# Kernel optimization log

Measured on AMD Instinct MI355X. Metric: run time of the kernel, lower is better.

Reference implementation:

```python
import jax, jax.numpy as jnp
import numpy as np

NQ = 16  # nqubits
BATCH = 256

def _ry(t):
    # t: (...,) real angles -> (..., 2, 2) complex64 Ry(t)
    c = jnp.cos(t / 2).astype(jnp.complex64)
    s = jnp.sin(t / 2).astype(jnp.complex64)
    return jnp.stack([jnp.stack([c, -s], -1), jnp.stack([s, c], -1)], -2)

def _rz(t):
    # diag(e^{-i t/2}, e^{i t/2})
    e0 = jnp.exp(-0.5j * t.astype(jnp.complex64))
    e1 = jnp.exp(0.5j * t.astype(jnp.complex64))
    z = jnp.zeros_like(e0)
    return jnp.stack([jnp.stack([e0, z], -1), jnp.stack([z, e1], -1)], -2)

def _apply_1q(st, g, w):
    # st: (B, 2^n) complex, g: (2,2) or (B,2,2); wire w (0 = most significant, matching kron order)
    B = st.shape[0]
    x = st.reshape(B, 2 ** w, 2, -1)
    if g.ndim == 3:
        x = jnp.einsum('iab,ilbr->ilar', g, x)
    else:
        x = jnp.einsum('ab,ilbr->ilar', g, x)
    return x.reshape(B, -1)

def _apply_cnot(st, c, t, n):
    # CNOT(control=c, target=t): flip target bit where control bit == 1
    B = st.shape[0]
    x = st.reshape((B,) + (2,) * n)
    c_ax = c + 1
    ctrl0 = jnp.take(x, 0, axis=c_ax)
    ctrl1 = jnp.take(x, 1, axis=c_ax)
    t_ax = t + 1 if t < c else t  # target axis index after removing control axis
    ctrl1 = jnp.flip(ctrl1, axis=t_ax)  # flip along size-2 axis == Pauli-X
    x = jnp.stack([ctrl0, ctrl1], axis=c_ax)
    return x.reshape(B, -1)

def _yzy(st, w3, n):
    # per-qubit Ry(a) Rz(b) Ry(c); params laid out (n, 3) applied in order a, b, c
    p = w3.reshape(n, 3)
    g = jnp.einsum('nab,nbc,ncd->nad', _ry(p[:, 2]), _rz(p[:, 1]), _ry(p[:, 0]))
    for i in range(n):
        st = _apply_1q(st, g[i], i)
    return st

def _ring(st, step, n):
    # ring_of_cnot (step=1) / ring_of_cnot2 (step=2)
    for i in range(n):
        st = _apply_cnot(st, i, (i + step) % n, n)
    return st

def _forward(inputs, weight):
    B, n = inputs.shape
    # |0...0> initial state, batched
    st = jnp.zeros((B, 2 ** n), jnp.complex64).at[:, 0].set(1.0)
    # PauliEncoding with pauli='Y': Ry(inputs[:, i]) on wire i (batched gate)
    enc = _ry(inputs)  # (B, n, 2, 2)
    for i in range(n):
        st = _apply_1q(st, enc[:, i], i)
    # BasicEntangleLayer x2 = YZY + ring_of_cnot
    st = _yzy(st, weight[0 * n:3 * n], n); st = _ring(st, 1, n)
    st = _yzy(st, weight[3 * n:6 * n], n); st = _ring(st, 1, n)
    # YZY, ring_of_cnot2, YZY, ring_of_cnot2, YZY
    st = _yzy(st, weight[6 * n:9 * n], n); st = _ring(st, 2, n)
    st = _yzy(st, weight[9 * n:12 * n], n); st = _ring(st, 2, n)
    st = _yzy(st, weight[12 * n:15 * n], n)
    # <Z_i> = sum_probs(bit_i=0) - sum_probs(bit_i=1); output scaled by 4 as in original
    probs = st.real ** 2 + st.imag ** 2  # (B, 2^n) real
    z = []
    for i in range(n):
        p = probs.reshape(B, 2 ** i, 2, -1)
        z.append((p[:, :, 0, :] - p[:, :, 1, :]).sum(axis=(1, 2)))
    return jnp.stack(z, axis=1) * 4.0  # (B, n)

def setup_inputs() -> dict:
    key = jax.random.key(0)
    k1, k2 = jax.random.split(key)
    inputs = jax.random.uniform(k1, (BATCH, NQ), jnp.float32, 0.0, 2.0 * np.pi)
    weight = jax.random.uniform(k2, (15 * NQ,), jnp.float32, 0.0, 2.0 * np.pi)
    return {"inputs": inputs, "weight": weight}

def reference(inputs, weight):
    return _forward(inputs, weight)
```

## Files before the change

### kernel.cpp

```cpp
#include <hip/hip_runtime.h>
#include <hip/hip_fp16.h>
#include <utility>
#include <type_traits>


struct M16 { unsigned r[16]; };

constexpr M16 ident() { M16 m{}; for (int i = 0; i < 16; ++i) m.r[i] = 1u << i; return m; }

constexpr M16 ringm(int s) {
  M16 m = ident();
  for (int i = 15; i >= 0; --i) {
    int pc = 15 - i;
    int pt = 15 - ((i + s) & 15);
    m.r[pt] ^= m.r[pc];
  }
  return m;
}

constexpr M16 mmul(M16 A, M16 B) {
  M16 C{};
  for (int p = 0; p < 16; ++p) {
    unsigned v = 0;
    for (int q = 0; q < 16; ++q) if ((A.r[p] >> q) & 1u) v ^= B.r[q];
    C.r[p] = v;
  }
  return C;
}

constexpr M16 minv(M16 A) {
  M16 I = ident();
  for (int col = 0; col < 16; ++col) {
    int piv = -1;
    for (int row = col; row < 16; ++row) if ((A.r[row] >> col) & 1u) { piv = row; break; }
    unsigned t = A.r[piv]; A.r[piv] = A.r[col]; A.r[col] = t;
    t = I.r[piv]; I.r[piv] = I.r[col]; I.r[col] = t;
    for (int row = 0; row < 16; ++row)
      if (row != col && ((A.r[row] >> col) & 1u)) { A.r[row] ^= A.r[col]; I.r[row] ^= I.r[col]; }
  }
  return I;
}

constexpr bool meq(M16 a, M16 b) { for (int i = 0; i < 16; ++i) if (a.r[i] != b.r[i]) return false; return true; }
constexpr unsigned colmask(M16 P, int b) { unsigned m = 0; for (int p = 0; p < 16; ++p) m |= ((P.r[p] >> b) & 1u) << p; return m; }
constexpr int popc16(unsigned x) { int c = 0; for (int i = 0; i < 16; ++i) c += (x >> i) & 1; return c; }
constexpr int topbit_pow(unsigned x) { int b = 0; for (int i = 0; i < 16; ++i) if ((x >> i) & 1) b = i; return 1 << b; }

struct Tables { unsigned gm[64]; unsigned gc[64]; unsigned meas[16]; };

constexpr Tables make_tables() {
  Tables T{};
  M16 R1 = ringm(1), R2 = ringm(2);
  M16 P0 = R1;
  M16 P1 = mmul(R1, R1);
  M16 P2 = mmul(P1, R2);
  M16 P3 = mmul(P2, R2);
  M16 P[4] = { P0, P1, P2, P3 };
  for (int k = 0; k < 4; ++k) {
    M16 A = minv(P[k]);
    for (int b = 0; b < 16; ++b) {
      T.gm[k * 16 + b] = colmask(P[k], b);
      T.gc[k * 16 + b] = A.r[b];
    }
  }
  M16 A5 = minv(P[3]);
  for (int w = 0; w < 16; ++w) T.meas[w] = A5.r[15 - w];
  return T;
}

constexpr Tables TB = make_tables();

constexpr bool check_tables() {
  for (int g = 0; g < 64; ++g) if ((popc16(TB.gm[g] & TB.gc[g]) & 1) != 1) return false;
  if (!meq(mmul(ringm(1), minv(ringm(1))), ident())) return false;
  if (!meq(mmul(ringm(2), minv(ringm(2))), ident())) return false;
  return true;
}
static_assert(check_tables(), "GF(2) table inconsistency");
static_assert(sizeof(__half2) == 4, "half2 size");

template<int N, int I = 0, typename F>
__device__ __forceinline__ void sfor(F&& f) {
  if constexpr (I < N) {
    f(std::integral_constant<int, I>{});
    sfor<N, I + 1>(static_cast<F&&>(f));
  }
}

__device__ __forceinline__ int h2i(__half2 v) { return __builtin_bit_cast(int, v); }
__device__ __forceinline__ __half2 i2h(int v) { return __builtin_bit_cast(__half2, v); }
__device__ __forceinline__ unsigned h2u(__half2 v) { return __builtin_bit_cast(unsigned, v); }
__device__ __forceinline__ __half2 u2h(unsigned v) { return __builtin_bit_cast(__half2, v); }

__device__ __forceinline__ __half2 hswap(__half2 v) { __half2 r; r.x = v.y; r.y = v.x; return r; }

__device__ __forceinline__ __half2 updc(__half2 xs, __half2 xp, const __half2 (&s)[4]) {
  __half2 y = __hmul2(s[0], xs);
  y = __hfma2(s[1], hswap(xs), y);
  y = __hfma2(s[2], xp, y);
  y = __hfma2(s[3], hswap(xp), y);
  return y;
}
template<int T>
__device__ __forceinline__ __half2 upd(__half2 xs, __half2 xp,
                                       const __half2 (&s0)[4], const __half2 (&s1)[4]) {
  if constexpr (T) return updc(xs, xp, s1); else return updc(xs, xp, s0);
}

__device__ __forceinline__ void su2_coeffs(float a, float b, float c,
                                           float& are, float& aim, float& bre, float& bim) {
  float sapc, capc, samc, camc, sb, cb;
  __sincosf((a + c) * 0.5f, &sapc, &capc);
  __sincosf((a - c) * 0.5f, &samc, &camc);
  __sincosf(b * 0.5f, &sb, &cb);
  are = cb * capc;
  aim = -sb * camc;
  bre = cb * sapc;
  bim = sb * samc;
}

__device__ __forceinline__ unsigned pkh2(float lo, float hi) {
  return h2u(__floats2half2_rn(lo, hi));
}

__device__ __forceinline__ float2 cmulf(float2 a, float vr, float vi) {
  return make_float2(a.x * vr - a.y * vi, a.x * vi + a.y * vr);
}

template<int G>
__device__ __forceinline__ void apply_gate(__half2 (&S)[64], unsigned tid,
                                           const unsigned* ctab, unsigned* xbuf) {
  constexpr unsigned m  = TB.gm[G];
  constexpr unsigned c  = TB.gc[G];
  constexpr unsigned mL = m & 63u;
  constexpr unsigned mT = m >> 6;
  constexpr unsigned mW = m >> 12;
  constexpr int      dt = popc16(c & mL) & 1;

  __half2 s0[4], s1[4];
  {
    const unsigned f = __popc((c >> 6) & tid) & 1u;
#pragma unroll
    for (int q = 0; q < 4; ++q) {
      const unsigned lo = ctab[G * 8 + q];
      const unsigned hi = ctab[G * 8 + 4 + q];
      s0[q] = u2h(f ? hi : lo);
      s1[q] = u2h(f ? lo : hi);
    }
  }

  if constexpr (mT == 0u) {
    static_assert(mT != 0u || dt == 1, "register-pair gate must flip role locally");
    constexpr int hb = topbit_pow(mL);
    sfor<32>([&](auto ii) {
      constexpr int i  = decltype(ii)::value;
      constexpr int L0 = ((i & ~(hb - 1)) << 1) | (i & (hb - 1));
      constexpr int L1 = L0 ^ (int)mL;
      constexpr int t  = popc16(c & (unsigned)L0) & 1;
      const __half2 x0 = S[L0], x1 = S[L1];
      S[L0] = upd<t>(x0, x1, s0, s1);
      S[L1] = upd<t ^ dt>(x1, x0, s0, s1);
    });
  } else if constexpr (mW == 0u) {
    if constexpr (mL == 0u) {
      sfor<64>([&](auto ll) {
        constexpr int L = decltype(ll)::value;
        constexpr int t = popc16(c & (unsigned)L) & 1;
        const __half2 xp = i2h(__shfl_xor(h2i(S[L]), (int)mT, 64));
        S[L] = upd<t>(S[L], xp, s0, s1);
      });
    } else {
      constexpr int hb = topbit_pow(mL);
      sfor<32>([&](auto ii) {
        constexpr int i  = decltype(ii)::value;
        constexpr int L0 = ((i & ~(hb - 1)) << 1) | (i & (hb - 1));
        constexpr int L1 = L0 ^ (int)mL;
        constexpr int t  = popc16(c & (unsigned)L0) & 1;
        const __half2 x0 = S[L0], x1 = S[L1];
        const __half2 xp0 = i2h(__shfl_xor(h2i(x1), (int)mT, 64));
        const __half2 xp1 = i2h(__shfl_xor(h2i(x0), (int)mT, 64));
        S[L0] = upd<t>(x0, xp0, s0, s1);
        S[L1] = upd<t ^ dt>(x1, xp1, s0, s1);
      });
    }
  } else {
    constexpr unsigned hc = mL >> 3;
    const unsigned ptid = tid ^ mT;
    if constexpr (hc == 0u) {
      sfor<4>([&](auto gg_) {
        constexpr int g = decltype(gg_)::value;
        sfor<16>([&](auto ss) {
          constexpr int s = decltype(ss)::value;
          xbuf[s * 1024 + tid] = h2u(S[g * 16 + s]);
        });
        __syncthreads();
        sfor<16>([&](auto ss) {
          constexpr int s    = decltype(ss)::value;
          constexpr int L    = g * 16 + s;
          constexpr int slot = (L ^ (int)mL) & 15;
          constexpr int t    = popc16(c & (unsigned)L) & 1;
          const __half2 xp = u2h(xbuf[slot * 1024 + ptid]);
          S[L] = upd<t>(S[L], xp, s0, s1);
        });
        __syncthreads();
      });
    } else {
      constexpr int tb = topbit_pow(hc);
      sfor<8>([&](auto cc) {
        constexpr int cA = decltype(cc)::value;
        if constexpr ((cA & tb) == 0) {
          constexpr int cB = cA ^ (int)hc;
          sfor<8>([&](auto ss) {
            constexpr int s = decltype(ss)::value;
            xbuf[s * 1024 + tid]       = h2u(S[cA * 8 + s]);
            xbuf[(8 + s) * 1024 + tid] = h2u(S[cB * 8 + s]);
          });
          __syncthreads();
          sfor<8>([&](auto ss) {
            constexpr int s = decltype(ss)::value;
            {
              constexpr int L    = cA * 8 + s;
              constexpr int slot = 8 + ((L ^ (int)mL) & 7);
              constexpr int t    = popc16(c & (unsigned)L) & 1;
              const __half2 xp = u2h(xbuf[slot * 1024 + ptid]);
              S[L] = upd<t>(S[L], xp, s0, s1);
            }
            {
              constexpr int L    = cB * 8 + s;
              constexpr int slot = (L ^ (int)mL) & 7;
              constexpr int t    = popc16(c & (unsigned)L) & 1;
              const __half2 xp = u2h(xbuf[slot * 1024 + ptid]);
              S[L] = upd<t>(S[L], xp, s0, s1);
            }
          });
          __syncthreads();
        }
      });
    }
  }
}

__global__ __launch_bounds__(1024, 4)
void qcir_kernel(const float* __restrict__ inputs, const float* __restrict__ weight,
                 float* __restrict__ out) {
  __shared__ unsigned xbuf[24 * 1024];
  __shared__ unsigned ctab[64 * 8];
  __shared__ float4   itab[16];
  __shared__ float    red[16 * 16];

  const unsigned tid = threadIdx.x;
  const unsigned b   = blockIdx.x;

  if (tid < 64) {
    const int g = (int)tid;
    const int k = g >> 4;
    const int bb = g & 15;
    const int w = 15 - bb;
    const int base = 48 * (k + 1) + 3 * w;
    float are, aim, bre, bim;
    su2_coeffs(weight[base], weight[base + 1], weight[base + 2], are, aim, bre, bim);
    ctab[g * 8 + 0] = pkh2(are, are);
    ctab[g * 8 + 1] = pkh2(-aim, aim);
    ctab[g * 8 + 2] = pkh2(-bre, -bre);
    ctab[g * 8 + 3] = pkh2(-bim, bim);
    ctab[g * 8 + 4] = pkh2(are, are);
    ctab[g * 8 + 5] = pkh2(aim, -aim);
    ctab[g * 8 + 6] = pkh2(bre, bre);
    ctab[g * 8 + 7] = pkh2(-bim, bim);
  } else if (tid < 80) {
    const int w = (int)tid - 64;
    const float a = weight[3 * w] + inputs[b * 16 + w];
    float are, aim, bre, bim;
    su2_coeffs(a, weight[3 * w + 1], weight[3 * w + 2], are, aim, bre, bim);
    itab[w] = make_float4(are, aim, bre, bim);
  }
  __syncthreads();

  __half2 S[64];
  float2 P = make_float2(1.f, 0.f);
#pragma unroll
  for (int p = 6; p <= 15; ++p) {
    const int bit = (int)(tid >> (p - 6)) & 1;
    const float4 t = itab[15 - p];
    P = cmulf(P, bit ? t.z : t.x, bit ? t.w : t.y);
  }
  sfor<8>([&](auto hh) {
    constexpr int h = decltype(hh)::value;
    float2 ph = P;
    sfor<3>([&](auto qq) {
      constexpr int q   = decltype(qq)::value;
      constexpr int bit = (h >> q) & 1;
      const float4 t = itab[15 - (3 + q)];
      if constexpr (bit) ph = cmulf(ph, t.z, t.w); else ph = cmulf(ph, t.x, t.y);
    });
    sfor<8>([&](auto ll) {
      constexpr int l = decltype(ll)::value;
      float2 pl = ph;
      sfor<3>([&](auto qq) {
        constexpr int q   = decltype(qq)::value;
        constexpr int bit = (l >> q) & 1;
        const float4 t = itab[15 - q];
        if constexpr (bit) pl = cmulf(pl, t.z, t.w); else pl = cmulf(pl, t.x, t.y);
      });
      S[h * 8 + l] = __floats2half2_rn(pl.x, pl.y);
    });
  });

  sfor<64>([&](auto gg) { apply_gate<decltype(gg)::value>(S, tid, ctab, xbuf); });

  float acc[16];
  sfor<16>([&](auto ww) { acc[decltype(ww)::value] = 0.f; });
  sfor<64>([&](auto ll) {
    constexpr int L = decltype(ll)::value;
    const float re = __low2float(S[L]);
    const float im = __high2float(S[L]);
    const float p = re * re + im * im;
    sfor<16>([&](auto ww) {
      constexpr int w = decltype(ww)::value;
      constexpr int t = popc16(TB.meas[w] & 63u & (unsigned)L) & 1;
      if constexpr (t) acc[w] -= p; else acc[w] += p;
    });
  });
  sfor<16>([&](auto ww) {
    constexpr int w = decltype(ww)::value;
    const unsigned fw = __popc((TB.meas[w] >> 6) & tid) & 1u;
    float z = fw ? -acc[w] : acc[w];
#pragma unroll
    for (int d = 1; d < 64; d <<= 1) z += __shfl_xor(z, d, 64);
    if ((tid & 63u) == 0u) red[(tid >> 6) * 16 + w] = z;
  });
  __syncthreads();
  if (tid < 16) {
    float s = 0.f;
#pragma unroll
    for (int v = 0; v < 16; ++v) s += red[v * 16 + tid];
    out[b * 16 + tid] = 4.f * s;
  }
}

extern "C" void kernel_launch(void* const* d_in, const int* in_sizes, int n_in,
                              void* d_out, int out_size, void* d_ws, size_t ws_size,
                              hipStream_t stream) {
  const float* inputs = (const float*)d_in[0];
  const float* weight = (const float*)d_in[1];
  float* out = (float*)d_out;
  const int B = in_sizes[0] / 16;
  qcir_kernel<<<B, 1024, 0, stream>>>(inputs, weight, out);
}
```

Baseline: 337.1 us.

## Split state between registers and LDS with compile-time qubit remapping

Each thread now keeps half its 64 amplitudes in registers and half in a resident LDS array. The split uses a compile-time permutation of qubits to physical bit positions, chosen greedily so most gates are local or touch only the LDS half. Cross-wave gates now read and update the partner amplitudes in place in LDS instead of staging them through an exchange buffer. This aims to cut register pressure and the exchange traffic, but adds LDS accesses to every gate and a barrier before most non-local gates. It also drops the occupancy hint in the launch bounds and halves the coefficient table by applying the sign flip with an XOR.

```diff
diff --git a/kernel.cpp b/kernel.cpp
--- a/kernel.cpp
+++ b/kernel.cpp
@@ -45,6 +45,7 @@
 constexpr unsigned colmask(M16 P, int b) { unsigned m = 0; for (int p = 0; p < 16; ++p) m |= ((P.r[p] >> b) & 1u) << p; return m; }
 constexpr int popc16(unsigned x) { int c = 0; for (int i = 0; i < 16; ++i) c += (x >> i) & 1; return c; }
 constexpr int topbit_pow(unsigned x) { int b = 0; for (int i = 0; i < 16; ++i) if ((x >> i) & 1) b = i; return 1 << b; }
+constexpr int ctzu(unsigned x) { for (int i = 0; i < 32; ++i) if ((x >> i) & 1) return i; return 32; }
 
 struct Tables { unsigned gm[64]; unsigned gc[64]; unsigned meas[16]; };
 
@@ -79,6 +80,104 @@
 static_assert(check_tables(), "GF(2) table inconsistency");
 static_assert(sizeof(__half2) == 4, "half2 size");
 
+struct Assign {
+  int hpos; unsigned wset, rset, lset;
+  int nbad;
+  int phys_of[16];
+  int orig_of[16];
+  unsigned pm[64], pc[64], pmeas[16];
+};
+
+constexpr Assign make_assign() {
+  Assign A{};
+  int bestBad = 1000, bh = -1; unsigned bw = 0;
+  for (int h = 0; h < 16; ++h) {
+    bool alive[64]; int nAlive = 0;
+    for (int g = 0; g < 64; ++g) {
+      alive[g] = ((TB.gm[g] >> h) & 1u) == 0u;
+      if (alive[g]) ++nAlive;
+    }
+    unsigned w = 0;
+    int covered = 0;
+    for (int pick = 0; pick < 4; ++pick) {
+      int bestP = -1, bestC = -1;
+      for (int p = 0; p < 16; ++p) {
+        if (p == h || ((w >> p) & 1u)) continue;
+        int cnt = 0;
+        for (int g = 0; g < 64; ++g)
+          if (alive[g] && ((TB.gm[g] >> p) & 1u)) ++cnt;
+        if (cnt > bestC) { bestC = cnt; bestP = p; }
+      }
+      w |= 1u << bestP;
+      for (int g = 0; g < 64; ++g)
+        if (alive[g] && ((TB.gm[g] >> bestP) & 1u)) { alive[g] = false; ++covered; }
+    }
+    int bad = covered;
+    if (bad < bestBad) { bestBad = bad; bh = h; bw = w; }
+  }
+  A.hpos = bh; A.wset = bw; A.nbad = bestBad;
+
+  unsigned rem = 0xFFFFu & ~bw & ~(1u << bh);
+  int pos[11] = {}; int np = 0;
+  for (int p = 0; p < 16; ++p) if ((rem >> p) & 1u) pos[np++] = p;
+  int bestLoc = -1; unsigned br = 0;
+  for (int a = 0; a < 11; ++a) for (int b = a + 1; b < 11; ++b)
+    for (int c = b + 1; c < 11; ++c) for (int d = c + 1; d < 11; ++d)
+      for (int e = d + 1; e < 11; ++e) {
+        unsigned r = (1u << pos[a]) | (1u << pos[b]) | (1u << pos[c]) | (1u << pos[d]) | (1u << pos[e]);
+        unsigned localset = r | (1u << bh);
+        int loc = 0;
+        for (int g = 0; g < 64; ++g) if ((TB.gm[g] & ~localset) == 0u) ++loc;
+        if (loc > bestLoc) { bestLoc = loc; br = r; }
+      }
+  A.rset = br; A.lset = rem & ~br;
+
+  int pr = 0, pl = 6, pw = 12;
+  for (int p = 0; p < 16; ++p) {
+    if ((A.rset >> p) & 1u)      { A.phys_of[p] = pr;  A.orig_of[pr]  = p; ++pr; }
+    else if (p == bh)            { A.phys_of[p] = 5;   A.orig_of[5]   = p; }
+    else if ((A.lset >> p) & 1u) { A.phys_of[p] = pl;  A.orig_of[pl]  = p; ++pl; }
+    else                         { A.phys_of[p] = pw;  A.orig_of[pw]  = p; ++pw; }
+  }
+  for (int g = 0; g < 64; ++g) {
+    unsigned m = 0, c = 0;
+    for (int p = 0; p < 16; ++p) {
+      if ((TB.gm[g] >> p) & 1u) m |= 1u << A.phys_of[p];
+      if ((TB.gc[g] >> p) & 1u) c |= 1u << A.phys_of[p];
+    }
+    A.pm[g] = m; A.pc[g] = c;
+  }
+  for (int w2 = 0; w2 < 16; ++w2) {
+    unsigned mm = 0;
+    for (int p = 0; p < 16; ++p) if ((TB.meas[w2] >> p) & 1u) mm |= 1u << A.phys_of[p];
+    A.pmeas[w2] = mm;
+  }
+  return A;
+}
+
+constexpr Assign AS = make_assign();
+
+constexpr bool check_assign() {
+  for (int g = 0; g < 64; ++g) if ((popc16(AS.pm[g] & AS.pc[g]) & 1) != 1) return false;
+  if (popc16(AS.rset) != 5 || popc16(AS.wset) != 4 || popc16(AS.lset) != 6) return false;
+  return true;
+}
+static_assert(check_assign(), "assignment inconsistency");
+
+struct RPlan { int stage[32]; int slot[32]; };
+constexpr RPlan make_rplan(unsigned mr) {
+  RPlan P{}; bool vis[32] = {};
+  int g = 0, sl = 0;
+  for (int r = 0; r < 32; ++r) if (!vis[r]) {
+    int p = r ^ (int)mr;
+    P.stage[r] = g; P.slot[r] = sl; vis[r] = true; ++sl;
+    if (p != r) { P.stage[p] = g; P.slot[p] = sl; vis[p] = true; ++sl; }
+    if (sl >= 4) { sl = 0; ++g; }
+  }
+  return P;
+}
+template<unsigned MR> constexpr RPlan rplan_v = make_rplan(MR);
+
 template<int N, int I = 0, typename F>
 __device__ __forceinline__ void sfor(F&& f) {
   if constexpr (I < N) {
@@ -94,17 +193,18 @@
 
 __device__ __forceinline__ __half2 hswap(__half2 v) { __half2 r; r.x = v.y; r.y = v.x; return r; }
 
-__device__ __forceinline__ __half2 updc(__half2 xs, __half2 xp, const __half2 (&s)[4]) {
-  __half2 y = __hmul2(s[0], xs);
-  y = __hfma2(s[1], hswap(xs), y);
-  y = __hfma2(s[2], xp, y);
+template<int T>
+__device__ __forceinline__ __half2 upd(__half2 x, __half2 xp, const __half2 (&s)[4]) {
+  __half2 y = __hmul2(s[0], x);
+  if constexpr (T) {
+    y = __hfma2(__hneg2(s[1]), hswap(x), y);
+    y = __hfma2(__hneg2(s[2]), xp, y);
+  } else {
+    y = __hfma2(s[1], hswap(x), y);
+    y = __hfma2(s[2], xp, y);
+  }
   y = __hfma2(s[3], hswap(xp), y);
   return y;
-}
-template<int T>
-__device__ __forceinline__ __half2 upd(__half2 xs, __half2 xp,
-                                       const __half2 (&s0)[4], const __half2 (&s1)[4]) {
-  if constexpr (T) return updc(xs, xp, s1); else return updc(xs, xp, s0);
 }
 
 __device__ __forceinline__ void su2_coeffs(float a, float b, float c,
@@ -128,123 +228,152 @@
 }
 
 template<int G>
-__device__ __forceinline__ void apply_gate(__half2 (&S)[64], unsigned tid,
-                                           const unsigned* ctab, unsigned* xbuf) {
-  constexpr unsigned m  = TB.gm[G];
-  constexpr unsigned c  = TB.gc[G];
-  constexpr unsigned mL = m & 63u;
-  constexpr unsigned mT = m >> 6;
-  constexpr unsigned mW = m >> 12;
-  constexpr int      dt = popc16(c & mL) & 1;
-
-  __half2 s0[4], s1[4];
-  {
-    const unsigned f = __popc((c >> 6) & tid) & 1u;
-#pragma unroll
-    for (int q = 0; q < 4; ++q) {
-      const unsigned lo = ctab[G * 8 + q];
-      const unsigned hi = ctab[G * 8 + 4 + q];
-      s0[q] = u2h(f ? hi : lo);
-      s1[q] = u2h(f ? lo : hi);
-    }
-  }
-
-  if constexpr (mT == 0u) {
-    static_assert(mT != 0u || dt == 1, "register-pair gate must flip role locally");
-    constexpr int hb = topbit_pow(mL);
-    sfor<32>([&](auto ii) {
-      constexpr int i  = decltype(ii)::value;
-      constexpr int L0 = ((i & ~(hb - 1)) << 1) | (i & (hb - 1));
-      constexpr int L1 = L0 ^ (int)mL;
-      constexpr int t  = popc16(c & (unsigned)L0) & 1;
-      const __half2 x0 = S[L0], x1 = S[L1];
-      S[L0] = upd<t>(x0, x1, s0, s1);
-      S[L1] = upd<t ^ dt>(x1, x0, s0, s1);
-    });
-  } else if constexpr (mW == 0u) {
-    if constexpr (mL == 0u) {
-      sfor<64>([&](auto ll) {
-        constexpr int L = decltype(ll)::value;
-        constexpr int t = popc16(c & (unsigned)L) & 1;
-        const __half2 xp = i2h(__shfl_xor(h2i(S[L]), (int)mT, 64));
-        S[L] = upd<t>(S[L], xp, s0, s1);
+__device__ __forceinline__ void apply_gate(__half2 (&R)[32], unsigned tid,
+                                           const unsigned* ctab, unsigned* ldsS,
+                                           unsigned* xbuf) {
+  constexpr unsigned m   = AS.pm[G];
+  constexpr unsigned c   = AS.pc[G];
+  constexpr unsigned mr  = m & 31u;
+  constexpr unsigned mh  = (m >> 5) & 1u;
+  constexpr unsigned mt  = (m >> 6) & 1023u;
+  constexpr unsigned mw  = m >> 12;
+  constexpr unsigned cr  = c & 31u;
+  constexpr unsigned chb = (c >> 5) & 1u;
+
+  const unsigned f  = __popc((c >> 6) & tid) & 1u;
+  const unsigned fm = f ? 0x80008000u : 0u;
+  __half2 s[4];
+  s[0] = u2h(ctab[G * 4 + 0]);
+  s[1] = u2h(ctab[G * 4 + 1] ^ fm);
+  s[2] = u2h(ctab[G * 4 + 2] ^ fm);
+  s[3] = u2h(ctab[G * 4 + 3]);
+
+  constexpr bool curLocal  = (m >> 6) == 0u;
+  constexpr bool prevLocal = (G == 0) ? true : ((AS.pm[G - 1] >> 6) == 0u);
+  if constexpr (!(curLocal && prevLocal)) __syncthreads();
+
+  if constexpr (mt == 0u) {
+    if constexpr (mh == 0u) {
+      constexpr int hb = topbit_pow(mr);
+      sfor<16>([&](auto ii) {
+        constexpr int i  = decltype(ii)::value;
+        constexpr int r0 = ((i & ~(hb - 1)) << 1) | (i & (hb - 1));
+        constexpr int r1 = r0 ^ (int)mr;
+        constexpr int t0 = popc16(cr & (unsigned)r0) & 1;
+        {
+          const __half2 x0 = R[r0], x1 = R[r1];
+          R[r0] = upd<t0>(x0, x1, s);
+          R[r1] = upd<t0 ^ 1>(x1, x0, s);
+        }
+        {
+          constexpr int tl = t0 ^ (int)chb;
+          const __half2 x0 = u2h(ldsS[r0 * 1024 + tid]);
+          const __half2 x1 = u2h(ldsS[r1 * 1024 + tid]);
+          ldsS[r0 * 1024 + tid] = h2u(upd<tl>(x0, x1, s));
+          ldsS[r1 * 1024 + tid] = h2u(upd<tl ^ 1>(x1, x0, s));
+        }
       });
     } else {
-      constexpr int hb = topbit_pow(mL);
-      sfor<32>([&](auto ii) {
-        constexpr int i  = decltype(ii)::value;
-        constexpr int L0 = ((i & ~(hb - 1)) << 1) | (i & (hb - 1));
-        constexpr int L1 = L0 ^ (int)mL;
-        constexpr int t  = popc16(c & (unsigned)L0) & 1;
-        const __half2 x0 = S[L0], x1 = S[L1];
-        const __half2 xp0 = i2h(__shfl_xor(h2i(x1), (int)mT, 64));
-        const __half2 xp1 = i2h(__shfl_xor(h2i(x0), (int)mT, 64));
-        S[L0] = upd<t>(x0, xp0, s0, s1);
-        S[L1] = upd<t ^ dt>(x1, xp1, s0, s1);
+      sfor<32>([&](auto rr) {
+        constexpr int r = decltype(rr)::value;
+        constexpr int t = popc16(cr & (unsigned)r) & 1;
+        const __half2 x = R[r];
+        const __half2 y = u2h(ldsS[(r ^ (int)mr) * 1024 + tid]);
+        R[r] = upd<t>(x, y, s);
+        ldsS[(r ^ (int)mr) * 1024 + tid] = h2u(upd<t ^ 1>(y, x, s));
       });
     }
+  } else if constexpr (mh == 1u) {
+    const unsigned pt = tid ^ mt;
+    sfor<32>([&](auto rr) {
+      constexpr int r = decltype(rr)::value;
+      constexpr int t = popc16(cr & (unsigned)r) & 1;
+      const __half2 x = R[r];
+      const __half2 y = u2h(ldsS[(r ^ (int)mr) * 1024 + pt]);
+      R[r] = upd<t>(x, y, s);
+      ldsS[(r ^ (int)mr) * 1024 + pt] = h2u(upd<t ^ 1>(y, x, s));
+    });
   } else {
-    constexpr unsigned hc = mL >> 3;
-    const unsigned ptid = tid ^ mT;
-    if constexpr (hc == 0u) {
-      sfor<4>([&](auto gg_) {
-        constexpr int g = decltype(gg_)::value;
-        sfor<16>([&](auto ss) {
-          constexpr int s = decltype(ss)::value;
-          xbuf[s * 1024 + tid] = h2u(S[g * 16 + s]);
+    const unsigned pt = tid ^ mt;
+    if constexpr (mr != 0u) {
+      constexpr int q = ctzu(mr);
+      sfor<32>([&](auto rr) {
+        constexpr int r = decltype(rr)::value;
+        if constexpr (((r >> q) & 1) == 0) {
+          constexpr int r2 = r ^ (int)mr;
+          constexpr int t  = (popc16(cr & (unsigned)r) & 1) ^ (int)chb;
+          const __half2 x = u2h(ldsS[r * 1024 + tid]);
+          const __half2 y = u2h(ldsS[r2 * 1024 + pt]);
+          ldsS[r * 1024 + tid] = h2u(upd<t>(x, y, s));
+          ldsS[r2 * 1024 + pt] = h2u(upd<t ^ 1>(y, x, s));
+        }
+      });
+    } else {
+      const unsigned po = (tid >> ctzu(mt)) & 1u;
+      sfor<32>([&](auto rr) {
+        constexpr int r  = decltype(rr)::value;
+        constexpr int r4 = (r >> 4) & 1;
+        constexpr int t  = (popc16(cr & (unsigned)r) & 1) ^ (int)chb;
+        if (po == (unsigned)r4) {
+          const __half2 x = u2h(ldsS[r * 1024 + tid]);
+          const __half2 y = u2h(ldsS[r * 1024 + pt]);
+          ldsS[r * 1024 + tid] = h2u(upd<t>(x, y, s));
+          ldsS[r * 1024 + pt]  = h2u(upd<t ^ 1>(y, x, s));
+        }
+      });
+    }
+    if constexpr (mw == 0u) {
+      if constexpr (mr == 0u) {
+        sfor<32>([&](auto rr) {
+          constexpr int r = decltype(rr)::value;
+          constexpr int t = popc16(cr & (unsigned)r) & 1;
+          const __half2 xp = i2h(__shfl_xor(h2i(R[r]), (int)mt, 64));
+          R[r] = upd<t>(R[r], xp, s);
+        });
+      } else {
+        constexpr int hb = topbit_pow(mr);
+        constexpr int dt = popc16(cr & mr) & 1;
+        sfor<16>([&](auto ii) {
+          constexpr int i  = decltype(ii)::value;
+          constexpr int r0 = ((i & ~(hb - 1)) << 1) | (i & (hb - 1));
+          constexpr int r1 = r0 ^ (int)mr;
+          constexpr int t  = popc16(cr & (unsigned)r0) & 1;
+          const __half2 x0 = R[r0], x1 = R[r1];
+          const __half2 xp0 = i2h(__shfl_xor(h2i(x1), (int)mt, 64));
+          const __half2 xp1 = i2h(__shfl_xor(h2i(x0), (int)mt, 64));
+          R[r0] = upd<t>(x0, xp0, s);
+          R[r1] = upd<t ^ dt>(x1, xp1, s);
+        });
+      }
+    } else {
+      sfor<8>([&](auto gi) {
+        constexpr int gidx = decltype(gi)::value;
+        sfor<32>([&](auto rr) {
+          constexpr int r = decltype(rr)::value;
+          if constexpr (rplan_v<mr>.stage[r] == gidx)
+            xbuf[rplan_v<mr>.slot[r] * 1024 + tid] = h2u(R[r]);
         });
         __syncthreads();
-        sfor<16>([&](auto ss) {
-          constexpr int s    = decltype(ss)::value;
-          constexpr int L    = g * 16 + s;
-          constexpr int slot = (L ^ (int)mL) & 15;
-          constexpr int t    = popc16(c & (unsigned)L) & 1;
-          const __half2 xp = u2h(xbuf[slot * 1024 + ptid]);
-          S[L] = upd<t>(S[L], xp, s0, s1);
+        sfor<32>([&](auto rr) {
+          constexpr int r = decltype(rr)::value;
+          if constexpr (rplan_v<mr>.stage[r] == gidx) {
+            constexpr int t = popc16(cr & (unsigned)r) & 1;
+            const __half2 xp = u2h(xbuf[rplan_v<mr>.slot[r ^ (int)mr] * 1024 + pt]);
+            R[r] = upd<t>(R[r], xp, s);
+          }
         });
         __syncthreads();
       });
-    } else {
-      constexpr int tb = topbit_pow(hc);
-      sfor<8>([&](auto cc) {
-        constexpr int cA = decltype(cc)::value;
-        if constexpr ((cA & tb) == 0) {
-          constexpr int cB = cA ^ (int)hc;
-          sfor<8>([&](auto ss) {
-            constexpr int s = decltype(ss)::value;
-            xbuf[s * 1024 + tid]       = h2u(S[cA * 8 + s]);
-            xbuf[(8 + s) * 1024 + tid] = h2u(S[cB * 8 + s]);
-          });
-          __syncthreads();
-          sfor<8>([&](auto ss) {
-            constexpr int s = decltype(ss)::value;
-            {
-              constexpr int L    = cA * 8 + s;
-              constexpr int slot = 8 + ((L ^ (int)mL) & 7);
-              constexpr int t    = popc16(c & (unsigned)L) & 1;
-              const __half2 xp = u2h(xbuf[slot * 1024 + ptid]);
-              S[L] = upd<t>(S[L], xp, s0, s1);
-            }
-            {
-              constexpr int L    = cB * 8 + s;
-              constexpr int slot = (L ^ (int)mL) & 7;
-              constexpr int t    = popc16(c & (unsigned)L) & 1;
-              const __half2 xp = u2h(xbuf[slot * 1024 + ptid]);
-              S[L] = upd<t>(S[L], xp, s0, s1);
-            }
-          });
-          __syncthreads();
-        }
-      });
-    }
-  }
-}
-
-__global__ __launch_bounds__(1024, 4)
+    }
+  }
+}
+
+__global__ __launch_bounds__(1024)
 void qcir_kernel(const float* __restrict__ inputs, const float* __restrict__ weight,
                  float* __restrict__ out) {
-  __shared__ unsigned xbuf[24 * 1024];
-  __shared__ unsigned ctab[64 * 8];
+  __shared__ unsigned ldsS[32 * 1024];
+  __shared__ unsigned xbuf[4 * 1024];
+  __shared__ unsigned ctab[64 * 4];
   __shared__ float4   itab[16];
   __shared__ float    red[16 * 16];
 
@@ -252,21 +381,17 @@
   const unsigned b   = blockIdx.x;
 
   if (tid < 64) {
-    const int g = (int)tid;
-    const int k = g >> 4;
+    const int g  = (int)tid;
+    const int k  = g >> 4;
     const int bb = g & 15;
-    const int w = 15 - bb;
+    const int w  = 15 - bb;
     const int base = 48 * (k + 1) + 3 * w;
     float are, aim, bre, bim;
     su2_coeffs(weight[base], weight[base + 1], weight[base + 2], are, aim, bre, bim);
-    ctab[g * 8 + 0] = pkh2(are, are);
-    ctab[g * 8 + 1] = pkh2(-aim, aim);
-    ctab[g * 8 + 2] = pkh2(-bre, -bre);
-    ctab[g * 8 + 3] = pkh2(-bim, bim);
-    ctab[g * 8 + 4] = pkh2(are, are);
-    ctab[g * 8 + 5] = pkh2(aim, -aim);
-    ctab[g * 8 + 6] = pkh2(bre, bre);
-    ctab[g * 8 + 7] = pkh2(-bim, bim);
+    ctab[g * 4 + 0] = pkh2(are, are);
+    ctab[g * 4 + 1] = pkh2(-aim, aim);
+    ctab[g * 4 + 2] = pkh2(-bre, -bre);
+    ctab[g * 4 + 3] = pkh2(-bim, bim);
   } else if (tid < 80) {
     const int w = (int)tid - 64;
     const float a = weight[3 * w] + inputs[b * 16 + w];
@@ -276,54 +401,63 @@
   }
   __syncthreads();
 
-  __half2 S[64];
-  float2 P = make_float2(1.f, 0.f);
+  __half2 R[32];
+  float2 P0 = make_float2(1.f, 0.f);
 #pragma unroll
-  for (int p = 6; p <= 15; ++p) {
-    const int bit = (int)(tid >> (p - 6)) & 1;
-    const float4 t = itab[15 - p];
-    P = cmulf(P, bit ? t.z : t.x, bit ? t.w : t.y);
-  }
-  sfor<8>([&](auto hh) {
-    constexpr int h = decltype(hh)::value;
-    float2 ph = P;
-    sfor<3>([&](auto qq) {
+  for (int pp = 6; pp < 16; ++pp) {
+    const int bit = (int)(tid >> (pp - 6)) & 1;
+    const float4 tt = itab[15 - AS.orig_of[pp]];
+    P0 = cmulf(P0, bit ? tt.z : tt.x, bit ? tt.w : tt.y);
+  }
+  const float4 th = itab[15 - AS.orig_of[5]];
+  const float2 Ph0 = cmulf(P0, th.x, th.y);
+  const float2 Ph1 = cmulf(P0, th.z, th.w);
+  sfor<32>([&](auto rr) {
+    constexpr int r = decltype(rr)::value;
+    float2 v0 = Ph0, v1 = Ph1;
+    sfor<5>([&](auto qq) {
       constexpr int q   = decltype(qq)::value;
-      constexpr int bit = (h >> q) & 1;
-      const float4 t = itab[15 - (3 + q)];
-      if constexpr (bit) ph = cmulf(ph, t.z, t.w); else ph = cmulf(ph, t.x, t.y);
+      constexpr int bit = (r >> q) & 1;
+      const float4 tq = itab[15 - AS.orig_of[q]];
+      if constexpr (bit) { v0 = cmulf(v0, tq.z, tq.w); v1 = cmulf(v1, tq.z, tq.w); }
+      else               { v0 = cmulf(v0, tq.x, tq.y); v1 = cmulf(v1, tq.x, tq.y); }
     });
-    sfor<8>([&](auto ll) {
-      constexpr int l = decltype(ll)::value;
-      float2 pl = ph;
-      sfor<3>([&](auto qq) {
-        constexpr int q   = decltype(qq)::value;
-        constexpr int bit = (l >> q) & 1;
-        const float4 t = itab[15 - q];
-        if constexpr (bit) pl = cmulf(pl, t.z, t.w); else pl = cmulf(pl, t.x, t.y);
-      });
-      S[h * 8 + l] = __floats2half2_rn(pl.x, pl.y);
-    });
+    R[r] = __floats2half2_rn(v0.x, v0.y);
+    ldsS[r * 1024 + tid] = h2u(__floats2half2_rn(v1.x, v1.y));
   });
 
-  sfor<64>([&](auto gg) { apply_gate<decltype(gg)::value>(S, tid, ctab, xbuf); });
-
+  sfor<64>([&](auto gg) { apply_gate<decltype(gg)::value>(R, tid, ctab, ldsS, xbuf); });
+
+  __syncthreads();
   float acc[16];
   sfor<16>([&](auto ww) { acc[decltype(ww)::value] = 0.f; });
-  sfor<64>([&](auto ll) {
-    constexpr int L = decltype(ll)::value;
-    const float re = __low2float(S[L]);
-    const float im = __high2float(S[L]);
+  sfor<32>([&](auto rr) {
+    constexpr int r = decltype(rr)::value;
+    const float re = __low2float(R[r]);
+    const float im = __high2float(R[r]);
     const float p = re * re + im * im;
     sfor<16>([&](auto ww) {
       constexpr int w = decltype(ww)::value;
-      constexpr int t = popc16(TB.meas[w] & 63u & (unsigned)L) & 1;
+      constexpr int t = popc16(AS.pmeas[w] & 31u & (unsigned)r) & 1;
+      if constexpr (t) acc[w] -= p; else acc[w] += p;
+    });
+  });
+  sfor<32>([&](auto rr) {
+    constexpr int r = decltype(rr)::value;
+    const __half2 v = u2h(ldsS[r * 1024 + tid]);
+    const float re = __low2float(v);
+    const float im = __high2float(v);
+    const float p = re * re + im * im;
+    sfor<16>([&](auto ww) {
+      constexpr int w = decltype(ww)::value;
+      constexpr int t = (popc16(AS.pmeas[w] & 31u & (unsigned)r) & 1) ^
+                        (int)((AS.pmeas[w] >> 5) & 1u);
       if constexpr (t) acc[w] -= p; else acc[w] += p;
     });
   });
   sfor<16>([&](auto ww) {
     constexpr int w = decltype(ww)::value;
-    const unsigned fw = __popc((TB.meas[w] >> 6) & tid) & 1u;
+    const unsigned fw = __popc((AS.pmeas[w] >> 6) & tid) & 1u;
     float z = fw ? -acc[w] : acc[w];
 #pragma unroll
     for (int d = 1; d < 64; d <<= 1) z += __shfl_xor(z, d, 64);
@@ -331,10 +465,10 @@
   });
   __syncthreads();
   if (tid < 16) {
-    float s = 0.f;
+    float sum = 0.f;
 #pragma unroll
-    for (int v = 0; v < 16; ++v) s += red[v * 16 + tid];
-    out[b * 16 + tid] = 4.f * s;
+    for (int v = 0; v < 16; ++v) sum += red[v * 16 + tid];
+    out[b * 16 + tid] = 4.f * sum;
   }
 }
 
```

After: 692.1 us. +105.3%, slower.
